# Kernel tuning notes

Hardware: AMD Instinct MI355X
Metric: run time of the kernel (lower is better)

Reference implementation:

```python
import jax, jax.numpy as jnp
import numpy as np

HIDDEN = 4096
HEADS = 32
HEAD_DIM = 128
MEM_FREQ = 63
MAX_MEM = 16  # hardcoded max_mem_cnt in landmark_grouped_softmax
NEG = jnp.finfo(jnp.float32).min


def rotate_half(x):
    x1, x2 = jnp.split(x, 2, axis=-1)
    return jnp.concatenate((-x2, x1), axis=-1)


def rope_tables(seq_len, dim, base=10000.0):
    inv_freq = 1.0 / (base ** (jnp.arange(0, dim, 2, dtype=jnp.float32) / dim))
    t = jnp.arange(seq_len, dtype=jnp.float32)
    freqs = jnp.einsum('i,j->ij', t, inv_freq)
    emb = jnp.concatenate((freqs, freqs), axis=-1)  # [seq, dim]
    return jnp.cos(emb), jnp.sin(emb)


def landmark_grouped_softmax(x, is_mem, last_section_mask):
    # x: [b,h,q,k] fp32; is_mem/last_section_mask: bool [1,1,q,k]
    full_access = is_mem | last_section_mask
    mem_group_idx = jnp.cumsum(is_mem.astype(jnp.int32), axis=-1)
    # resp = where(last, 15, where(is_mem, 15, cumsum)) == where(full_access, 15, cumsum)
    resp = jnp.where(full_access, MAX_MEM - 1, mem_group_idx)  # [1,1,q,k]
    # scatter_reduce(amax, include_self=False) + gather -> per-position group max
    maxes = jnp.full(x.shape, NEG, dtype=x.dtype)
    for g in range(MAX_MEM):
        m = resp == g
        gmax = jnp.max(jnp.where(m, x, NEG), axis=-1, keepdims=True)
        maxes = jnp.where(m, gmax, maxes)
    x_exp = jnp.exp((x - maxes).astype(jnp.float32))
    # scatter_add + gather -> per-position group denom
    denom = jnp.zeros_like(x_exp)
    for g in range(MAX_MEM):
        m = resp == g
        gsum = jnp.sum(jnp.where(m, x_exp, 0.0), axis=-1, keepdims=True)
        denom = jnp.where(m, gsum, denom)
    probs = x_exp / denom
    # group_prob scatter at where(is_mem, cumsum-1, 15); gathered at resp only where
    # not full_access (resp = cumsum = g selects landmark whose cumsum == g+1)
    lm_prob = jnp.zeros_like(probs)
    for g in range(MAX_MEM - 1):
        landmark = is_mem & (mem_group_idx == g + 1)
        gp = jnp.sum(jnp.where(landmark, probs, 0.0), axis=-1, keepdims=True)
        sel = (~full_access) & (mem_group_idx == g)
        lm_prob = jnp.where(sel, gp, lm_prob)
    mult = jnp.where(full_access, last_section_mask.astype(probs.dtype), lm_prob)
    return probs * mult


def setup_inputs() -> dict:
    key = jax.random.key(0)
    k0, k1, k2, k3, k4 = jax.random.split(key, 5)
    B, Q = 2, 960
    scale = 1.0 / np.sqrt(HIDDEN).astype(np.float32)
    hidden_states = jax.random.normal(k0, (B, Q, HIDDEN), jnp.float32) * 0.02
    wq = jax.random.normal(k1, (HIDDEN, HIDDEN), jnp.float32) * scale
    wk = jax.random.normal(k2, (HIDDEN, HIDDEN), jnp.float32) * scale
    wv = jax.random.normal(k3, (HIDDEN, HIDDEN), jnp.float32) * scale
    wo = jax.random.normal(k4, (HIDDEN, HIDDEN), jnp.float32) * scale
    idx = jnp.arange(Q)
    block = idx // (MEM_FREQ + 1)
    is_mem = jnp.broadcast_to((((idx + 1) % (MEM_FREQ + 1)) == 0)[None, None, None, :], (1, 1, Q, Q))
    last_section_mask = (block[None, :] == block[:, None])[None, None]
    causal = idx[None, :] <= idx[:, None]
    attention_mask = jnp.where(causal, 0.0, NEG)[None, None].astype(jnp.float32)
    position_ids = jnp.arange(Q, dtype=jnp.int32)[None]
    return {"hidden_states": hidden_states, "wq": wq, "wk": wk, "wv": wv, "wo": wo,
            "attention_mask": attention_mask, "position_ids": position_ids,
            "is_mem": is_mem, "last_section_mask": last_section_mask}


def reference(hidden_states, wq, wk, wv, wo, attention_mask, position_ids, is_mem, last_section_mask):
    b, q_len, _ = hidden_states.shape
    def split_heads(t):
        return t.reshape(b, q_len, HEADS, HEAD_DIM).transpose(0, 2, 1, 3)  # [b,h,q,d]
    qs = split_heads(hidden_states @ wq)
    ks = split_heads(hidden_states @ wk)
    vs = split_heads(hidden_states @ wv)
    cos_t, sin_t = rope_tables(q_len, HEAD_DIM)
    cos = cos_t[position_ids][:, None]  # [1,1,q,d]
    sin = sin_t[position_ids][:, None]
    qs = qs * cos + rotate_half(qs) * sin
    ks = ks * cos + rotate_half(ks) * sin
    aw = jnp.einsum('bhqd,bhkd->bhqk', qs, ks) / np.sqrt(HEAD_DIM).astype(np.float32)
    aw = jnp.maximum(aw + attention_mask, NEG)
    probs = landmark_grouped_softmax(aw, is_mem, last_section_mask)
    out = jnp.einsum('bhqk,bhkd->bhqd', probs, vs)
    out = out.transpose(0, 2, 1, 3).reshape(b, q_len, HIDDEN)
    return out @ wo
```

## Files before the change

kernel.cpp:

```cpp
#include <hip/hip_runtime.h>

typedef _Float16 h8v __attribute__((ext_vector_type(8)));
typedef _Float16 h4v __attribute__((ext_vector_type(4)));
typedef float f4v __attribute__((ext_vector_type(4)));

#define NEGF (-3.4028234663852886e38f)

static __device__ __forceinline__ void gload16(const void* g, void* l) {
  __builtin_amdgcn_global_load_lds((const __attribute__((address_space(1))) void*)g,
                                   (__attribute__((address_space(3))) void*)l, 16, 0, 0);
}

__global__ __launch_bounds__(256) void cast_hs_kernel(const float* __restrict__ in,
                                                      _Float16* __restrict__ out) {
  int i = (blockIdx.x * 256 + threadIdx.x) * 4;
  float4 v = *(const float4*)(in + i);
  h4v o = {(_Float16)v.x, (_Float16)v.y, (_Float16)v.z, (_Float16)v.w};
  *(h4v*)(out + i) = o;
}

__global__ __launch_bounds__(256) void wtrans_kernel(const float* __restrict__ W,
                                                     _Float16* __restrict__ Wt) {
  __shared__ float tile[32][33];
  int tx = threadIdx.x & 31, ty = threadIdx.x >> 5;
  int c0 = blockIdx.x * 32;
  int r0 = blockIdx.y * 32;
  for (int i = 0; i < 4; i++)
    tile[ty + i * 8][tx] = W[(size_t)(r0 + ty + i * 8) * 4096 + c0 + tx];
  __syncthreads();
  for (int i = 0; i < 4; i++)
    Wt[(size_t)(c0 + ty + i * 8) * 4096 + r0 + tx] = (_Float16)tile[tx][ty + i * 8];
}

template <typename OutT, bool HEAD_LAYOUT>
__global__ __launch_bounds__(256) void gemm_kernel(const _Float16* __restrict__ A,
                                                   const _Float16* __restrict__ Bt,
                                                   OutT* __restrict__ C) {
  const int K = 4096, N = 4096;
  int m0 = blockIdx.y * 128, n0 = blockIdx.x * 128;
  __shared__ __align__(16) _Float16 As[4096];
  __shared__ __align__(16) _Float16 Bs[4096];
  int t = threadIdx.x;
  int lane = t & 63, w = t >> 6, quad = lane >> 4, l16 = lane & 15;
  int wm = (w >> 1) * 64, wn = (w & 1) * 64;
  f4v acc[4][4] = {};
  int c_a = t >> 7;
  int mr = t & 127;
  const _Float16* Arow0 = A + (size_t)(m0 + mr) * K + c_a * 8;
  const _Float16* Arow1 = Arow0 + 16;
  const _Float16* Brow0 = Bt + (size_t)(n0 + mr) * K + c_a * 8;
  const _Float16* Brow1 = Brow0 + 16;
  for (int kk = 0; kk < K; kk += 32) {
    __syncthreads();
    gload16(Arow0 + kk, As + t * 8);
    gload16(Arow1 + kk, As + (t + 256) * 8);
    gload16(Brow0 + kk, Bs + t * 8);
    gload16(Brow1 + kk, Bs + (t + 256) * 8);
    __syncthreads();
    h8v af[4], bf[4];
    for (int mi = 0; mi < 4; mi++)
      af[mi] = *(const h8v*)(As + (quad * 128 + wm + mi * 16 + l16) * 8);
    for (int ni = 0; ni < 4; ni++)
      bf[ni] = *(const h8v*)(Bs + (quad * 128 + wn + ni * 16 + l16) * 8);
    for (int mi = 0; mi < 4; mi++)
      for (int ni = 0; ni < 4; ni++)
        acc[mi][ni] = __builtin_amdgcn_mfma_f32_16x16x32_f16(af[mi], bf[ni], acc[mi][ni], 0, 0, 0);
  }
  for (int mi = 0; mi < 4; mi++)
    for (int ni = 0; ni < 4; ni++) {
      int col = n0 + wn + ni * 16 + l16;
      for (int rr = 0; rr < 4; rr++) {
        int row = m0 + wm + mi * 16 + quad * 4 + rr;
        size_t oidx;
        if (HEAD_LAYOUT) {
          int b = row >= 960 ? 1 : 0;
          int q = row - b * 960;
          oidx = ((size_t)(b * 32 + (col >> 7)) * 960 + q) * 128 + (col & 127);
        } else {
          oidx = (size_t)row * N + col;
        }
        C[oidx] = (OutT)acc[mi][ni][rr];
      }
    }
}

__global__ __launch_bounds__(256) void rope_kernel(_Float16* __restrict__ x) {
  int idx = blockIdx.x * 256 + threadIdx.x;
  int d = idx & 63;
  int rest = idx >> 6;
  int q = rest % 960;
  size_t base = (size_t)rest * 128 + d;
  float x1 = (float)x[base], x2 = (float)x[base + 64];
  float invf = exp2f((float)d * -0.20762050593046016f);
  float ang = (float)q * invf;
  float c = cosf(ang), s = sinf(ang);
  x[base]      = (_Float16)(x1 * c - x2 * s);
  x[base + 64] = (_Float16)(x2 * c + x1 * s);
}

__global__ __launch_bounds__(256) void vtrans_kernel(const _Float16* __restrict__ in,
                                                     _Float16* __restrict__ vt) {
  __shared__ _Float16 tile[32][33];
  int tx = threadIdx.x & 31, ty = threadIdx.x >> 5;
  int q0 = blockIdx.x * 32;
  int d0 = blockIdx.y * 32;
  int bh = blockIdx.z;
  for (int i = 0; i < 4; i++)
    tile[ty + i * 8][tx] = in[((size_t)bh * 960 + q0 + ty + i * 8) * 128 + d0 + tx];
  __syncthreads();
  for (int i = 0; i < 4; i++)
    vt[((size_t)bh * 128 + d0 + ty + i * 8) * 960 + q0 + tx] = tile[tx][ty + i * 8];
}

__global__ __launch_bounds__(256) void attn_kernel(const _Float16* __restrict__ qr,
                                                   const _Float16* __restrict__ kr,
                                                   const _Float16* __restrict__ vt,
                                                   _Float16* __restrict__ attn_out) {
  const int qt = blockIdx.x;
  const int bh = blockIdx.y;
  const int b = bh >> 5, h = bh & 31;
  const int q0 = qt * 16;
  const int qb = q0 >> 6;
  const int t = threadIdx.x;
  const int w = t >> 6, lane = t & 63, quad = lane >> 4, l16 = lane & 15;

  __shared__ __align__(16) float S[16][964];
  __shared__ float Mg[16][16];
  __shared__ float Dg[16][16];
  __shared__ float Wg[16][16];

  const _Float16* qbase = qr + (size_t)(bh * 960 + q0) * 128;
  h8v qf[4];
  for (int dc = 0; dc < 4; dc++)
    qf[dc] = *(const h8v*)(qbase + l16 * 128 + dc * 32 + quad * 8);

  const float rscale = 0.08838834764831845f;
  for (int kt = 0; kt <= qb; kt++) {
    int kc0 = kt * 64 + w * 16;
    const _Float16* kbase = kr + (size_t)(bh * 960 + kc0 + l16) * 128;
    f4v acc = {0.f, 0.f, 0.f, 0.f};
    for (int dc = 0; dc < 4; dc++) {
      h8v kf = *(const h8v*)(kbase + dc * 32 + quad * 8);
      acc = __builtin_amdgcn_mfma_f32_16x16x32_f16(qf[dc], kf, acc, 0, 0, 0);
    }
    int kcol = kc0 + l16;
    for (int r = 0; r < 4; r++) {
      int m = quad * 4 + r;
      S[m][kcol] = (kcol <= q0 + m) ? acc[r] * rscale : NEGF;
    }
  }
  __syncthreads();

  const int ng = qb + 1;
  for (int p = w; p < 16 * ng; p += 4) {
    int r = p & 15, gi = p >> 4;
    if (gi == qb) {
      float v1 = S[r][qb * 64 + lane];
      float v2 = (lane < qb) ? S[r][lane * 64 + 63] : NEGF;
      float mx = fmaxf(v1, v2);
      for (int m = 32; m; m >>= 1) mx = fmaxf(mx, __shfl_xor(mx, m));
      float e = __expf(v1 - mx) + ((lane < qb) ? __expf(v2 - mx) : 0.f);
      for (int m = 32; m; m >>= 1) e += __shfl_xor(e, m);
      if (lane == 0) { Mg[r][15] = mx; Dg[r][15] = e; }
    } else {
      float v1 = (lane < 63) ? S[r][gi * 64 + lane] : NEGF;
      float mx = v1;
      for (int m = 32; m; m >>= 1) mx = fmaxf(mx, __shfl_xor(mx, m));
      float e = (lane < 63) ? __expf(v1 - mx) : 0.f;
      for (int m = 32; m; m >>= 1) e += __shfl_xor(e, m);
      if (lane == 0) { Mg[r][gi] = mx; Dg[r][gi] = e; }
    }
  }
  __syncthreads();

  {
    int r = t & 15, g = t >> 4;
    if (g < qb)
      Wg[r][g] = __expf(S[r][g * 64 + 63] - Mg[r][15]) / (Dg[r][15] * Dg[r][g]);
    else if (g == 15)
      Wg[r][15] = 1.f / Dg[r][15];
  }
  __syncthreads();

  for (int p = w; p < 16 * ng; p += 4) {
    int r = p & 15, g = p >> 4;
    int k = g * 64 + lane;
    float s = S[r][k];
    float wgt;
    if (g == qb)           wgt = __expf(s - Mg[r][15]) * Wg[r][15];
    else if (lane == 63)   wgt = 0.f;
    else                   wgt = __expf(s - Mg[r][g]) * Wg[r][g];
    S[r][k] = wgt;
  }
  __syncthreads();

  {
    int d0 = w * 32;
    const _Float16* vbase = vt + (size_t)(bh * 128 + d0) * 960;
    f4v oacc[2] = {{0.f, 0.f, 0.f, 0.f}, {0.f, 0.f, 0.f, 0.f}};
    int nkc = (qb + 1) * 2;
    for (int kc = 0; kc < nkc; kc++) {
      int k0 = kc * 32 + quad * 8;
      float4 wa = *(const float4*)&S[l16][k0];
      float4 wb = *(const float4*)&S[l16][k0 + 4];
      h8v af = {(_Float16)wa.x, (_Float16)wa.y, (_Float16)wa.z, (_Float16)wa.w,
                (_Float16)wb.x, (_Float16)wb.y, (_Float16)wb.z, (_Float16)wb.w};
      for (int nt = 0; nt < 2; nt++) {
        h8v bfv = *(const h8v*)(vbase + (nt * 16 + l16) * 960 + k0);
        oacc[nt] = __builtin_amdgcn_mfma_f32_16x16x32_f16(af, bfv, oacc[nt], 0, 0, 0);
      }
    }
    for (int nt = 0; nt < 2; nt++)
      for (int rr = 0; rr < 4; rr++) {
        int qrow = q0 + quad * 4 + rr;
        int col = h * 128 + d0 + nt * 16 + l16;
        attn_out[(size_t)(b * 960 + qrow) * 4096 + col] = (_Float16)oacc[nt][rr];
      }
  }
}

extern "C" void kernel_launch(void* const* d_in, const int* in_sizes, int n_in,
                              void* d_out, int out_size, void* d_ws, size_t ws_size,
                              hipStream_t stream) {
  (void)in_sizes; (void)n_in; (void)out_size; (void)ws_size;
  const float* hs = (const float*)d_in[0];
  const float* wq = (const float*)d_in[1];
  const float* wk = (const float*)d_in[2];
  const float* wv = (const float*)d_in[3];
  const float* wo = (const float*)d_in[4];
  char* ws = (char*)d_ws;
  _Float16* wt   = (_Float16*)(ws);
  _Float16* hsf  = (_Float16*)(ws + 33554432ull);
  _Float16* qr   = (_Float16*)(ws + 49283072ull);
  _Float16* kr   = (_Float16*)(ws + 65011712ull);
  _Float16* vtmp = (_Float16*)(ws + 80740352ull);
  _Float16* vt   = (_Float16*)(ws + 96468992ull);
  _Float16* attn = hsf;
  float* out = (float*)d_out;

  hipLaunchKernelGGL(cast_hs_kernel, dim3(7680), dim3(256), 0, stream, hs, hsf);

  hipLaunchKernelGGL(wtrans_kernel, dim3(128, 128), dim3(256), 0, stream, wq, wt);
  hipLaunchKernelGGL((gemm_kernel<_Float16, true>), dim3(32, 15), dim3(256), 0, stream, hsf, wt, qr);
  hipLaunchKernelGGL(rope_kernel, dim3(15360), dim3(256), 0, stream, qr);
  hipLaunchKernelGGL(wtrans_kernel, dim3(128, 128), dim3(256), 0, stream, wk, wt);
  hipLaunchKernelGGL((gemm_kernel<_Float16, true>), dim3(32, 15), dim3(256), 0, stream, hsf, wt, kr);
  hipLaunchKernelGGL(rope_kernel, dim3(15360), dim3(256), 0, stream, kr);
  hipLaunchKernelGGL(wtrans_kernel, dim3(128, 128), dim3(256), 0, stream, wv, wt);
  hipLaunchKernelGGL((gemm_kernel<_Float16, true>), dim3(32, 15), dim3(256), 0, stream, hsf, wt, vtmp);
  hipLaunchKernelGGL(vtrans_kernel, dim3(30, 4, 64), dim3(256), 0, stream, vtmp, vt);
  hipLaunchKernelGGL(attn_kernel, dim3(60, 64), dim3(256), 0, stream, qr, kr, vt, attn);
  hipLaunchKernelGGL(wtrans_kernel, dim3(128, 128), dim3(256), 0, stream, wo, wt);
  hipLaunchKernelGGL((gemm_kernel<float, false>), dim3(32, 15), dim3(256), 0, stream, attn, wt, out);
}
```

Measured before the change: 1.132 ms.

## Fuse QKV GEMMs, merge RoPE launches, and rewrite attention as register-resident two-pass

The Q, K and V projections run as one GEMM launch over a concatenated transposed weight buffer when the workspace is large enough, and RoPE for Q and K runs in a single launch. The attention kernel is rewritten so each block handles 64 query rows with one wave per 16 rows. Group max and sum statistics are computed in registers through shuffles in a first pass, and QK^T is recomputed in a second pass that feeds per-wave fp16 probability tiles straight into the PV MFMAs. This removes the large fp32 score buffer in shared memory and its block-wide barriers, at the cost of computing QK twice and needing more workspace for the fused path.

```diff
diff --git a/kernel.cpp b/kernel.cpp
--- a/kernel.cpp
+++ b/kernel.cpp
@@ -32,23 +32,18 @@
     Wt[(size_t)(c0 + ty + i * 8) * 4096 + r0 + tx] = (_Float16)tile[tx][ty + i * 8];
 }
 
-template <typename OutT, bool HEAD_LAYOUT>
-__global__ __launch_bounds__(256) void gemm_kernel(const _Float16* __restrict__ A,
-                                                   const _Float16* __restrict__ Bt,
-                                                   OutT* __restrict__ C) {
-  const int K = 4096, N = 4096;
-  int m0 = blockIdx.y * 128, n0 = blockIdx.x * 128;
-  __shared__ __align__(16) _Float16 As[4096];
-  __shared__ __align__(16) _Float16 Bs[4096];
+static __device__ __forceinline__ void gemm_mainloop(const _Float16* __restrict__ A,
+                                                     const _Float16* __restrict__ Bt,
+                                                     _Float16* As, _Float16* Bs,
+                                                     f4v (&acc)[4][4]) {
+  const int K = 4096;
   int t = threadIdx.x;
   int lane = t & 63, w = t >> 6, quad = lane >> 4, l16 = lane & 15;
   int wm = (w >> 1) * 64, wn = (w & 1) * 64;
-  f4v acc[4][4] = {};
-  int c_a = t >> 7;
-  int mr = t & 127;
-  const _Float16* Arow0 = A + (size_t)(m0 + mr) * K + c_a * 8;
+  int c_a = t >> 7, mr = t & 127;
+  const _Float16* Arow0 = A + (size_t)mr * K + c_a * 8;
   const _Float16* Arow1 = Arow0 + 16;
-  const _Float16* Brow0 = Bt + (size_t)(n0 + mr) * K + c_a * 8;
+  const _Float16* Brow0 = Bt + (size_t)mr * K + c_a * 8;
   const _Float16* Brow1 = Brow0 + 16;
   for (int kk = 0; kk < K; kk += 32) {
     __syncthreads();
@@ -66,25 +61,81 @@
       for (int ni = 0; ni < 4; ni++)
         acc[mi][ni] = __builtin_amdgcn_mfma_f32_16x16x32_f16(af[mi], bf[ni], acc[mi][ni], 0, 0, 0);
   }
+}
+
+__global__ __launch_bounds__(256) void gemm_qkv_kernel(const _Float16* __restrict__ A,
+                                                       const _Float16* __restrict__ W3,
+                                                       _Float16* __restrict__ qr,
+                                                       _Float16* __restrict__ kr,
+                                                       _Float16* __restrict__ vtmp) {
+  __shared__ __align__(16) _Float16 As[4096];
+  __shared__ __align__(16) _Float16 Bs[4096];
+  int which = blockIdx.x % 3;
+  int n0 = (blockIdx.x / 3) * 128;
+  int m0 = blockIdx.y * 128;
+  const _Float16* Bt = W3 + (size_t)which * 16777216 + (size_t)n0 * 4096;
+  _Float16* C = which == 0 ? qr : (which == 1 ? kr : vtmp);
+  f4v acc[4][4] = {};
+  gemm_mainloop(A + (size_t)m0 * 4096, Bt, As, Bs, acc);
+  int t = threadIdx.x, lane = t & 63, w = t >> 6, quad = lane >> 4, l16 = lane & 15;
+  int wm = (w >> 1) * 64, wn = (w & 1) * 64;
   for (int mi = 0; mi < 4; mi++)
     for (int ni = 0; ni < 4; ni++) {
       int col = n0 + wn + ni * 16 + l16;
       for (int rr = 0; rr < 4; rr++) {
         int row = m0 + wm + mi * 16 + quad * 4 + rr;
-        size_t oidx;
-        if (HEAD_LAYOUT) {
-          int b = row >= 960 ? 1 : 0;
-          int q = row - b * 960;
-          oidx = ((size_t)(b * 32 + (col >> 7)) * 960 + q) * 128 + (col & 127);
-        } else {
-          oidx = (size_t)row * N + col;
-        }
-        C[oidx] = (OutT)acc[mi][ni][rr];
-      }
-    }
-}
-
-__global__ __launch_bounds__(256) void rope_kernel(_Float16* __restrict__ x) {
+        int bb = row >= 960 ? 1 : 0;
+        int q = row - bb * 960;
+        C[((size_t)(bb * 32 + (col >> 7)) * 960 + q) * 128 + (col & 127)] = (_Float16)acc[mi][ni][rr];
+      }
+    }
+}
+
+__global__ __launch_bounds__(256) void gemm_head_kernel(const _Float16* __restrict__ A,
+                                                        const _Float16* __restrict__ Bt,
+                                                        _Float16* __restrict__ C) {
+  __shared__ __align__(16) _Float16 As[4096];
+  __shared__ __align__(16) _Float16 Bs[4096];
+  int n0 = blockIdx.x * 128, m0 = blockIdx.y * 128;
+  f4v acc[4][4] = {};
+  gemm_mainloop(A + (size_t)m0 * 4096, Bt + (size_t)n0 * 4096, As, Bs, acc);
+  int t = threadIdx.x, lane = t & 63, w = t >> 6, quad = lane >> 4, l16 = lane & 15;
+  int wm = (w >> 1) * 64, wn = (w & 1) * 64;
+  for (int mi = 0; mi < 4; mi++)
+    for (int ni = 0; ni < 4; ni++) {
+      int col = n0 + wn + ni * 16 + l16;
+      for (int rr = 0; rr < 4; rr++) {
+        int row = m0 + wm + mi * 16 + quad * 4 + rr;
+        int bb = row >= 960 ? 1 : 0;
+        int q = row - bb * 960;
+        C[((size_t)(bb * 32 + (col >> 7)) * 960 + q) * 128 + (col & 127)] = (_Float16)acc[mi][ni][rr];
+      }
+    }
+}
+
+__global__ __launch_bounds__(256) void gemm_o_kernel(const _Float16* __restrict__ A,
+                                                     const _Float16* __restrict__ Bt,
+                                                     float* __restrict__ Cout) {
+  __shared__ __align__(16) _Float16 As[4096];
+  __shared__ __align__(16) _Float16 Bs[4096];
+  int n0 = blockIdx.x * 128, m0 = blockIdx.y * 128;
+  f4v acc[4][4] = {};
+  gemm_mainloop(A + (size_t)m0 * 4096, Bt + (size_t)n0 * 4096, As, Bs, acc);
+  int t = threadIdx.x, lane = t & 63, w = t >> 6, quad = lane >> 4, l16 = lane & 15;
+  int wm = (w >> 1) * 64, wn = (w & 1) * 64;
+  for (int mi = 0; mi < 4; mi++)
+    for (int ni = 0; ni < 4; ni++) {
+      int col = n0 + wn + ni * 16 + l16;
+      for (int rr = 0; rr < 4; rr++) {
+        int row = m0 + wm + mi * 16 + quad * 4 + rr;
+        Cout[(size_t)row * 4096 + col] = acc[mi][ni][rr];
+      }
+    }
+}
+
+__global__ __launch_bounds__(256) void rope2_kernel(_Float16* __restrict__ qx,
+                                                    _Float16* __restrict__ kx) {
+  _Float16* x = blockIdx.y ? kx : qx;
   int idx = blockIdx.x * 256 + threadIdx.x;
   int d = idx & 63;
   int rest = idx >> 6;
@@ -119,137 +170,176 @@
   const int qt = blockIdx.x;
   const int bh = blockIdx.y;
   const int b = bh >> 5, h = bh & 31;
-  const int q0 = qt * 16;
-  const int qb = q0 >> 6;
+  const int q0 = qt * 64;
   const int t = threadIdx.x;
   const int w = t >> 6, lane = t & 63, quad = lane >> 4, l16 = lane & 15;
-
-  __shared__ __align__(16) float S[16][964];
-  __shared__ float Mg[16][16];
-  __shared__ float Dg[16][16];
-  __shared__ float Wg[16][16];
-
-  const _Float16* qbase = qr + (size_t)(bh * 960 + q0) * 128;
+  const int lquad = lane & 48;
+
+  __shared__ __align__(16) _Float16 P[4][16][72];
+
+  const float rscale = 0.08838834764831845f;
+  const int r0 = q0 + w * 16;
+
+  const _Float16* qptr = qr + (size_t)(bh * 960 + r0 + l16) * 128 + quad * 8;
   h8v qf[4];
-  for (int dc = 0; dc < 4; dc++)
-    qf[dc] = *(const h8v*)(qbase + l16 * 128 + dc * 32 + quad * 8);
-
-  const float rscale = 0.08838834764831845f;
-  for (int kt = 0; kt <= qb; kt++) {
-    int kc0 = kt * 64 + w * 16;
-    const _Float16* kbase = kr + (size_t)(bh * 960 + kc0 + l16) * 128;
-    f4v acc = {0.f, 0.f, 0.f, 0.f};
-    for (int dc = 0; dc < 4; dc++) {
-      h8v kf = *(const h8v*)(kbase + dc * 32 + quad * 8);
-      acc = __builtin_amdgcn_mfma_f32_16x16x32_f16(qf[dc], kf, acc, 0, 0, 0);
-    }
-    int kcol = kc0 + l16;
-    for (int r = 0; r < 4; r++) {
-      int m = quad * 4 + r;
-      S[m][kcol] = (kcol <= q0 + m) ? acc[r] * rscale : NEGF;
-    }
-  }
-  __syncthreads();
-
-  const int ng = qb + 1;
-  for (int p = w; p < 16 * ng; p += 4) {
-    int r = p & 15, gi = p >> 4;
-    if (gi == qb) {
-      float v1 = S[r][qb * 64 + lane];
-      float v2 = (lane < qb) ? S[r][lane * 64 + 63] : NEGF;
-      float mx = fmaxf(v1, v2);
-      for (int m = 32; m; m >>= 1) mx = fmaxf(mx, __shfl_xor(mx, m));
-      float e = __expf(v1 - mx) + ((lane < qb) ? __expf(v2 - mx) : 0.f);
-      for (int m = 32; m; m >>= 1) e += __shfl_xor(e, m);
-      if (lane == 0) { Mg[r][15] = mx; Dg[r][15] = e; }
+  for (int dc = 0; dc < 4; dc++) qf[dc] = *(const h8v*)(qptr + dc * 32);
+
+  float sM[4], sD[4], sL[4], Wmul[4];
+  float Mcur[4], Dcur[4], M15[4], iD15[4];
+
+  for (int g = 0; g <= qt; g++) {
+    f4v acc[4];
+    for (int ct = 0; ct < 4; ct++) {
+      const _Float16* kptr = kr + (size_t)(bh * 960 + g * 64 + ct * 16 + l16) * 128 + quad * 8;
+      f4v a = {0.f, 0.f, 0.f, 0.f};
+      for (int dc = 0; dc < 4; dc++)
+        a = __builtin_amdgcn_mfma_f32_16x16x32_f16(qf[dc], *(const h8v*)(kptr + dc * 32), a, 0, 0, 0);
+      for (int rr = 0; rr < 4; rr++) acc[ct][rr] = a[rr] * rscale;
+    }
+    if (g < qt) {
+      for (int rr = 0; rr < 4; rr++) {
+        float s3 = acc[3][rr];
+        float mx = fmaxf(fmaxf(acc[0][rr], acc[1][rr]), acc[2][rr]);
+        if (l16 != 15) mx = fmaxf(mx, s3);
+        for (int m = 8; m; m >>= 1) mx = fmaxf(mx, __shfl_xor(mx, m));
+        float e = __expf(acc[0][rr] - mx) + __expf(acc[1][rr] - mx) + __expf(acc[2][rr] - mx);
+        if (l16 != 15) e += __expf(s3 - mx);
+        for (int m = 8; m; m >>= 1) e += __shfl_xor(e, m);
+        float slm = __shfl(s3, lquad + 15);
+        if (l16 == g) { sM[rr] = mx; sD[rr] = e; sL[rr] = slm; }
+      }
     } else {
-      float v1 = (lane < 63) ? S[r][gi * 64 + lane] : NEGF;
-      float mx = v1;
-      for (int m = 32; m; m >>= 1) mx = fmaxf(mx, __shfl_xor(mx, m));
-      float e = (lane < 63) ? __expf(v1 - mx) : 0.f;
-      for (int m = 32; m; m >>= 1) e += __shfl_xor(e, m);
-      if (lane == 0) { Mg[r][gi] = mx; Dg[r][gi] = e; }
-    }
-  }
-  __syncthreads();
-
-  {
-    int r = t & 15, g = t >> 4;
-    if (g < qb)
-      Wg[r][g] = __expf(S[r][g * 64 + 63] - Mg[r][15]) / (Dg[r][15] * Dg[r][g]);
-    else if (g == 15)
-      Wg[r][15] = 1.f / Dg[r][15];
-  }
-  __syncthreads();
-
-  for (int p = w; p < 16 * ng; p += 4) {
-    int r = p & 15, g = p >> 4;
-    int k = g * 64 + lane;
-    float s = S[r][k];
-    float wgt;
-    if (g == qb)           wgt = __expf(s - Mg[r][15]) * Wg[r][15];
-    else if (lane == 63)   wgt = 0.f;
-    else                   wgt = __expf(s - Mg[r][g]) * Wg[r][g];
-    S[r][k] = wgt;
-  }
-  __syncthreads();
-
-  {
-    int d0 = w * 32;
-    const _Float16* vbase = vt + (size_t)(bh * 128 + d0) * 960;
-    f4v oacc[2] = {{0.f, 0.f, 0.f, 0.f}, {0.f, 0.f, 0.f, 0.f}};
-    int nkc = (qb + 1) * 2;
-    for (int kc = 0; kc < nkc; kc++) {
-      int k0 = kc * 32 + quad * 8;
-      float4 wa = *(const float4*)&S[l16][k0];
-      float4 wb = *(const float4*)&S[l16][k0 + 4];
-      h8v af = {(_Float16)wa.x, (_Float16)wa.y, (_Float16)wa.z, (_Float16)wa.w,
-                (_Float16)wb.x, (_Float16)wb.y, (_Float16)wb.z, (_Float16)wb.w};
-      for (int nt = 0; nt < 2; nt++) {
-        h8v bfv = *(const h8v*)(vbase + (nt * 16 + l16) * 960 + k0);
-        oacc[nt] = __builtin_amdgcn_mfma_f32_16x16x32_f16(af, bfv, oacc[nt], 0, 0, 0);
-      }
-    }
-    for (int nt = 0; nt < 2; nt++)
-      for (int rr = 0; rr < 4; rr++) {
-        int qrow = q0 + quad * 4 + rr;
-        int col = h * 128 + d0 + nt * 16 + l16;
-        attn_out[(size_t)(b * 960 + qrow) * 4096 + col] = (_Float16)oacc[nt][rr];
-      }
-  }
+      for (int rr = 0; rr < 4; rr++) {
+        int row = r0 + quad * 4 + rr;
+        float v0 = (q0 + 0 * 16 + l16 <= row) ? acc[0][rr] : NEGF;
+        float v1 = (q0 + 1 * 16 + l16 <= row) ? acc[1][rr] : NEGF;
+        float v2 = (q0 + 2 * 16 + l16 <= row) ? acc[2][rr] : NEGF;
+        float v3 = (q0 + 3 * 16 + l16 <= row) ? acc[3][rr] : NEGF;
+        float mx = fmaxf(fmaxf(v0, v1), fmaxf(v2, v3));
+        for (int m = 8; m; m >>= 1) mx = fmaxf(mx, __shfl_xor(mx, m));
+        float e = 0.f;
+        if (v0 > -1e38f) e += __expf(v0 - mx);
+        if (v1 > -1e38f) e += __expf(v1 - mx);
+        if (v2 > -1e38f) e += __expf(v2 - mx);
+        if (v3 > -1e38f) e += __expf(v3 - mx);
+        for (int m = 8; m; m >>= 1) e += __shfl_xor(e, m);
+        Mcur[rr] = mx; Dcur[rr] = e;
+      }
+    }
+  }
+
+  for (int rr = 0; rr < 4; rr++) {
+    float vlm = (l16 < qt) ? sL[rr] : NEGF;
+    float ml = vlm;
+    for (int m = 8; m; m >>= 1) ml = fmaxf(ml, __shfl_xor(ml, m));
+    float m15 = fmaxf(Mcur[rr], ml);
+    float es = (l16 < qt) ? __expf(sL[rr] - m15) : 0.f;
+    float sum = es;
+    for (int m = 8; m; m >>= 1) sum += __shfl_xor(sum, m);
+    float d15 = Dcur[rr] * __expf(Mcur[rr] - m15) + sum;
+    M15[rr] = m15;
+    iD15[rr] = 1.f / d15;
+    Wmul[rr] = es * iD15[rr] / sD[rr];
+  }
+
+  f4v oacc[8] = {};
+  for (int g = 0; g <= qt; g++) {
+    f4v acc[4];
+    for (int ct = 0; ct < 4; ct++) {
+      const _Float16* kptr = kr + (size_t)(bh * 960 + g * 64 + ct * 16 + l16) * 128 + quad * 8;
+      f4v a = {0.f, 0.f, 0.f, 0.f};
+      for (int dc = 0; dc < 4; dc++)
+        a = __builtin_amdgcn_mfma_f32_16x16x32_f16(qf[dc], *(const h8v*)(kptr + dc * 32), a, 0, 0, 0);
+      for (int rr = 0; rr < 4; rr++) acc[ct][rr] = a[rr] * rscale;
+    }
+    float bM[4], bW[4];
+    if (g < qt)
+      for (int rr = 0; rr < 4; rr++) {
+        bM[rr] = __shfl(sM[rr], lquad + g);
+        bW[rr] = __shfl(Wmul[rr], lquad + g);
+      }
+    for (int ct = 0; ct < 4; ct++)
+      for (int rr = 0; rr < 4; rr++) {
+        float wgt;
+        if (g == qt) {
+          int col = q0 + ct * 16 + l16;
+          int row = r0 + quad * 4 + rr;
+          wgt = (col <= row) ? __expf(acc[ct][rr] - M15[rr]) * iD15[rr] : 0.f;
+        } else {
+          wgt = (ct == 3 && l16 == 15) ? 0.f : __expf(acc[ct][rr] - bM[rr]) * bW[rr];
+        }
+        P[w][quad * 4 + rr][ct * 16 + l16] = (_Float16)wgt;
+      }
+    __builtin_amdgcn_wave_barrier();
+    for (int c = 0; c < 2; c++) {
+      h8v af = *(const h8v*)&P[w][l16][c * 32 + quad * 8];
+      const _Float16* vbase = vt + (size_t)bh * 122880 + (size_t)(g * 64 + c * 32 + quad * 8);
+      for (int dt = 0; dt < 8; dt++) {
+        const _Float16* vptr = vbase + (size_t)(dt * 16 + l16) * 960;
+        oacc[dt] = __builtin_amdgcn_mfma_f32_16x16x32_f16(af, *(const h8v*)vptr, oacc[dt], 0, 0, 0);
+      }
+    }
+    __builtin_amdgcn_wave_barrier();
+  }
+
+  _Float16* obase = attn_out + (size_t)(b * 960 + r0 + quad * 4) * 4096 + h * 128 + l16;
+  for (int dt = 0; dt < 8; dt++)
+    for (int rr = 0; rr < 4; rr++)
+      obase[(size_t)rr * 4096 + dt * 16] = (_Float16)oacc[dt][rr];
 }
 
 extern "C" void kernel_launch(void* const* d_in, const int* in_sizes, int n_in,
                               void* d_out, int out_size, void* d_ws, size_t ws_size,
                               hipStream_t stream) {
-  (void)in_sizes; (void)n_in; (void)out_size; (void)ws_size;
+  (void)in_sizes; (void)n_in; (void)out_size;
   const float* hs = (const float*)d_in[0];
   const float* wq = (const float*)d_in[1];
   const float* wk = (const float*)d_in[2];
   const float* wv = (const float*)d_in[3];
   const float* wo = (const float*)d_in[4];
   char* ws = (char*)d_ws;
-  _Float16* wt   = (_Float16*)(ws);
-  _Float16* hsf  = (_Float16*)(ws + 33554432ull);
-  _Float16* qr   = (_Float16*)(ws + 49283072ull);
-  _Float16* kr   = (_Float16*)(ws + 65011712ull);
-  _Float16* vtmp = (_Float16*)(ws + 80740352ull);
-  _Float16* vt   = (_Float16*)(ws + 96468992ull);
-  _Float16* attn = hsf;
   float* out = (float*)d_out;
 
-  hipLaunchKernelGGL(cast_hs_kernel, dim3(7680), dim3(256), 0, stream, hs, hsf);
-
-  hipLaunchKernelGGL(wtrans_kernel, dim3(128, 128), dim3(256), 0, stream, wq, wt);
-  hipLaunchKernelGGL((gemm_kernel<_Float16, true>), dim3(32, 15), dim3(256), 0, stream, hsf, wt, qr);
-  hipLaunchKernelGGL(rope_kernel, dim3(15360), dim3(256), 0, stream, qr);
-  hipLaunchKernelGGL(wtrans_kernel, dim3(128, 128), dim3(256), 0, stream, wk, wt);
-  hipLaunchKernelGGL((gemm_kernel<_Float16, true>), dim3(32, 15), dim3(256), 0, stream, hsf, wt, kr);
-  hipLaunchKernelGGL(rope_kernel, dim3(15360), dim3(256), 0, stream, kr);
-  hipLaunchKernelGGL(wtrans_kernel, dim3(128, 128), dim3(256), 0, stream, wv, wt);
-  hipLaunchKernelGGL((gemm_kernel<_Float16, true>), dim3(32, 15), dim3(256), 0, stream, hsf, wt, vtmp);
-  hipLaunchKernelGGL(vtrans_kernel, dim3(30, 4, 64), dim3(256), 0, stream, vtmp, vt);
-  hipLaunchKernelGGL(attn_kernel, dim3(60, 64), dim3(256), 0, stream, qr, kr, vt, attn);
-  hipLaunchKernelGGL(wtrans_kernel, dim3(128, 128), dim3(256), 0, stream, wo, wt);
-  hipLaunchKernelGGL((gemm_kernel<float, false>), dim3(32, 15), dim3(256), 0, stream, attn, wt, out);
-}
+  if (ws_size >= 212860928ull) {
+    _Float16* wt3  = (_Float16*)(ws);
+    _Float16* wto  = (_Float16*)(ws + 100663296ull);
+    _Float16* hsf  = (_Float16*)(ws + 134217728ull);
+    _Float16* qr   = (_Float16*)(ws + 149946368ull);
+    _Float16* kr   = (_Float16*)(ws + 165675008ull);
+    _Float16* vtmp = (_Float16*)(ws + 181403648ull);
+    _Float16* vt   = (_Float16*)(ws + 197132288ull);
+    _Float16* attn = hsf;
+
+    hipLaunchKernelGGL(cast_hs_kernel, dim3(7680), dim3(256), 0, stream, hs, hsf);
+    hipLaunchKernelGGL(wtrans_kernel, dim3(128, 128), dim3(256), 0, stream, wq, wt3);
+    hipLaunchKernelGGL(wtrans_kernel, dim3(128, 128), dim3(256), 0, stream, wk, wt3 + 16777216);
+    hipLaunchKernelGGL(wtrans_kernel, dim3(128, 128), dim3(256), 0, stream, wv, wt3 + 33554432);
+    hipLaunchKernelGGL(wtrans_kernel, dim3(128, 128), dim3(256), 0, stream, wo, wto);
+    hipLaunchKernelGGL(gemm_qkv_kernel, dim3(96, 15), dim3(256), 0, stream, hsf, wt3, qr, kr, vtmp);
+    hipLaunchKernelGGL(rope2_kernel, dim3(15360, 2), dim3(256), 0, stream, qr, kr);
+    hipLaunchKernelGGL(vtrans_kernel, dim3(30, 4, 64), dim3(256), 0, stream, vtmp, vt);
+    hipLaunchKernelGGL(attn_kernel, dim3(15, 64), dim3(256), 0, stream, qr, kr, vt, attn);
+    hipLaunchKernelGGL(gemm_o_kernel, dim3(32, 15), dim3(256), 0, stream, attn, wto, out);
+  } else {
+    _Float16* wt   = (_Float16*)(ws);
+    _Float16* hsf  = (_Float16*)(ws + 33554432ull);
+    _Float16* qr   = (_Float16*)(ws + 49283072ull);
+    _Float16* kr   = (_Float16*)(ws + 65011712ull);
+    _Float16* vtmp = (_Float16*)(ws + 80740352ull);
+    _Float16* vt   = (_Float16*)(ws + 96468992ull);
+    _Float16* attn = hsf;
+
+    hipLaunchKernelGGL(cast_hs_kernel, dim3(7680), dim3(256), 0, stream, hs, hsf);
+    hipLaunchKernelGGL(wtrans_kernel, dim3(128, 128), dim3(256), 0, stream, wq, wt);
+    hipLaunchKernelGGL(gemm_head_kernel, dim3(32, 15), dim3(256), 0, stream, hsf, wt, qr);
+    hipLaunchKernelGGL(wtrans_kernel, dim3(128, 128), dim3(256), 0, stream, wk, wt);
+    hipLaunchKernelGGL(gemm_head_kernel, dim3(32, 15), dim3(256), 0, stream, hsf, wt, kr);
+    hipLaunchKernelGGL(rope2_kernel, dim3(15360, 2), dim3(256), 0, stream, qr, kr);
+    hipLaunchKernelGGL(wtrans_kernel, dim3(128, 128), dim3(256), 0, stream, wv, wt);
+    hipLaunchKernelGGL(gemm_head_kernel, dim3(32, 15), dim3(256), 0, stream, hsf, wt, vtmp);
+    hipLaunchKernelGGL(vtrans_kernel, dim3(30, 4, 64), dim3(256), 0, stream, vtmp, vt);
+    hipLaunchKernelGGL(attn_kernel, dim3(15, 64), dim3(256), 0, stream, qr, kr, vt, attn);
+    hipLaunchKernelGGL(wtrans_kernel, dim3(128, 128), dim3(256), 0, stream, wo, wt);
+    hipLaunchKernelGGL(gemm_o_kernel, dim3(32, 15), dim3(256), 0, stream, attn, wt, out);
+  }
+}
```

New measurement: 1.125 ms. No clear change (-0.6%).
